# Kernel tuning notes

Hardware: AMD Instinct MI355X
Metric: run time of the kernel (lower is better)

The kernel has to match this reference:

```python
import jax, jax.numpy as jnp
import numpy as np

NEG_INF = jnp.finfo(jnp.float32).min


def setup_inputs() -> dict:
    key = jax.random.key(0)
    ks = jax.random.split(key, 5)
    B, S, D = 2, 2048, 1024
    std = 0.02
    return {
        "x": jax.random.normal(ks[0], (B, S, D), dtype=jnp.float32),
        "attention_mask": jnp.ones((B, S), dtype=jnp.int32),
        "Wq": jax.random.normal(ks[1], (D, D), dtype=jnp.float32) * std,
        "Wk": jax.random.normal(ks[2], (D, D), dtype=jnp.float32) * std,
        "Wv": jax.random.normal(ks[3], (D, D), dtype=jnp.float32) * std,
        "Wo": jax.random.normal(ks[4], (D, D), dtype=jnp.float32) * std,
    }


def reference(x, attention_mask, Wq, Wk, Wv, Wo):
    B, S, D = x.shape
    H = 16
    Hd = D // H
    scale = jnp.float32(np.sqrt(Hd))

    # F.linear uses W @ x^T, i.e. x @ W.T
    def proj(x, W):
        return jnp.einsum('bsd,ed->bse', x, W).reshape(B, S, H, Hd).transpose(0, 2, 1, 3)

    q = proj(x, Wq)  # [B,H,S,Hd]
    k = proj(x, Wk)
    v = proj(x, Wv)

    scores = jnp.einsum('bhqd,bhkd->bhqk', q, k) / scale  # [B,H,S,S]
    causal = jnp.triu(jnp.ones((S, S), dtype=bool), k=1)
    scores = jnp.where(causal[None, None, :, :], NEG_INF, scores)
    key_pad = (attention_mask == 0)[:, None, None, :]  # [B,1,1,S]
    scores = jnp.where(key_pad, NEG_INF, scores)

    attn = jax.nn.softmax(scores, axis=-1)
    out = jnp.einsum('bhqk,bhkd->bhqd', attn, v)  # [B,H,S,Hd]
    out = out.transpose(0, 2, 1, 3).reshape(B, S, D)
    return jnp.einsum('bsd,ed->bse', out, Wo)
```

## Files before the change

kernel.cpp:

```cpp
#include <hip/hip_runtime.h>
#include <hip/hip_bf16.h>

typedef __attribute__((ext_vector_type(8))) short bf16x8;
typedef __attribute__((ext_vector_type(4))) short bf16x4;
typedef __attribute__((ext_vector_type(4))) float f32x4;

#define LOG2E 1.4426950408889634f
#define MBIAS 11.541560327111707f
#define NEGF  -3.0e38f

__device__ __forceinline__ void gl_lds16(const void* g, void* l) {
  __builtin_amdgcn_global_load_lds((const __attribute__((address_space(1))) void*)g,
                                   (__attribute__((address_space(3))) void*)l, 16, 0, 0);
}

__device__ __forceinline__ ushort f2bu(float x) {
  __hip_bfloat16 h = __float2bfloat16(x);
  return *(ushort*)&h;
}

__device__ __forceinline__ unsigned int fbits(float x) {
  union { float f; unsigned int u; } c; c.f = x; return c.u;
}

__global__ __launch_bounds__(256)
void cast_all_k(const float* __restrict__ x, const float* __restrict__ a, const float* __restrict__ b,
                const float* __restrict__ c, const float* __restrict__ d,
                ushort* __restrict__ ox, ushort* __restrict__ oa, ushort* __restrict__ ob,
                ushort* __restrict__ oc, ushort* __restrict__ od) {
  int i = blockIdx.x * 256 + threadIdx.x;
  const float* src; ushort* dst; int j;
  if (i < 1048576) {
    src = x; dst = ox; j = i;
  } else {
    int k = i - 1048576;
    int wsel = k >> 18; j = k & 262143;
    src = wsel == 0 ? a : wsel == 1 ? b : wsel == 2 ? c : d;
    dst = wsel == 0 ? oa : wsel == 1 ? ob : wsel == 2 ? oc : od;
  }
  float4 f = ((const float4*)src)[j];
  ushort4 u;
  u.x = f2bu(f.x); u.y = f2bu(f.y); u.z = f2bu(f.z); u.w = f2bu(f.w);
  ((ushort4*)dst)[j] = u;
}

template<int OUT_BF16>
__device__ __forceinline__ void gemm_body(const ushort* __restrict__ A, const ushort* __restrict__ B,
                                          void* __restrict__ C, int N, int Kd, float scale,
                                          int bm, int bn, ushort (*As)[4096], ushort (*Bs)[4096]) {
  const int t  = threadIdx.x;
  const int l  = t & 63;
  const int w  = t >> 6;
  const int lr = l & 15, lg = l >> 4;
  const int wr = (w >> 1) * 64, wc = (w & 1) * 64;

  auto stage = [&](int buf, int ktE) {
    int idx = t, row = idx >> 2, ch = idx & 3;
    gl_lds16(A + (size_t)(bm + row) * Kd + ktE + ((ch ^ (row & 3)) * 8), &As[buf][idx * 8]);
    gl_lds16(B + (size_t)(bn + row) * Kd + ktE + ((ch ^ (row & 3)) * 8), &Bs[buf][idx * 8]);
    idx = t + 256; row = idx >> 2; ch = idx & 3;
    gl_lds16(A + (size_t)(bm + row) * Kd + ktE + ((ch ^ (row & 3)) * 8), &As[buf][idx * 8]);
    gl_lds16(B + (size_t)(bn + row) * Kd + ktE + ((ch ^ (row & 3)) * 8), &Bs[buf][idx * 8]);
  };

  f32x4 acc[4][4] = {};
  const int nK = Kd >> 5;

  stage(0, 0);
  stage(1, 32);
  int cur = 0;
  for (int k5 = 0; k5 < nK; ++k5) {
    if (k5 + 2 < nK) {
      int nb = cur + 2; if (nb >= 3) nb -= 3;
      stage(nb, (k5 + 2) << 5);
      asm volatile("s_waitcnt vmcnt(8)" ::: "memory");
    } else if (k5 + 1 < nK) {
      asm volatile("s_waitcnt vmcnt(4)" ::: "memory");
    } else {
      asm volatile("s_waitcnt vmcnt(0)" ::: "memory");
    }
    __builtin_amdgcn_s_barrier();

    bf16x8 af[4], bfr[4];
#pragma unroll
    for (int m = 0; m < 4; ++m) {
      int row = wr + m * 16 + lr;
      af[m] = *(const bf16x8*)&As[cur][row * 32 + ((lg ^ (row & 3)) << 3)];
    }
#pragma unroll
    for (int n = 0; n < 4; ++n) {
      int row = wc + n * 16 + lr;
      bfr[n] = *(const bf16x8*)&Bs[cur][row * 32 + ((lg ^ (row & 3)) << 3)];
    }
#pragma unroll
    for (int m = 0; m < 4; ++m)
#pragma unroll
      for (int n = 0; n < 4; ++n)
        acc[m][n] = __builtin_amdgcn_mfma_f32_16x16x32_bf16(af[m], bfr[n], acc[m][n], 0, 0, 0);

    __builtin_amdgcn_s_barrier();
    ++cur; if (cur >= 3) cur -= 3;
  }

#pragma unroll
  for (int m = 0; m < 4; ++m)
#pragma unroll
    for (int n = 0; n < 4; ++n)
#pragma unroll
      for (int j = 0; j < 4; ++j) {
        int row = bm + wr + m * 16 + lg * 4 + j;
        int col = bn + wc + n * 16 + lr;
        float v = acc[m][n][j] * scale;
        if (OUT_BF16) {
          ((ushort*)C)[(size_t)row * N + col] = f2bu(v);
        } else {
          ((float*)C)[(size_t)row * N + col] = v;
        }
      }
}

__global__ __launch_bounds__(256)
void gemm_qkv(const ushort* __restrict__ A, const ushort* __restrict__ Wq, const ushort* __restrict__ Wk,
              const ushort* __restrict__ Wv, ushort* __restrict__ Qo, ushort* __restrict__ Ko,
              ushort* __restrict__ Vo, int Kd) {
  __shared__ __attribute__((aligned(16))) ushort As[3][4096];
  __shared__ __attribute__((aligned(16))) ushort Bs[3][4096];
  int f = blockIdx.x;
  int xcd = f & 7, i = f >> 3;
  int bx = xcd * 4 + (i & 3);
  int by = i >> 2;
  int which = by >> 3;
  const ushort* B = which == 0 ? Wq : which == 1 ? Wk : Wv;
  ushort* C       = which == 0 ? Qo : which == 1 ? Ko : Vo;
  float scale = which == 0 ? 0.125f : 1.0f;
  gemm_body<1>(A, B, C, 1024, Kd, scale, bx * 128, (by & 7) * 128, As, Bs);
}

__global__ __launch_bounds__(256)
void gemm_out64(const ushort* __restrict__ A, const ushort* __restrict__ B, float* __restrict__ C,
                int N, int Kd) {
  __shared__ __attribute__((aligned(16))) ushort As[3][2048];
  __shared__ __attribute__((aligned(16))) ushort Bs[3][4096];
  const int t  = threadIdx.x;
  const int l  = t & 63;
  const int w  = t >> 6;
  const int lr = l & 15, lg = l >> 4;
  const int wr = (w >> 1) * 32, wc = (w & 1) * 64;
  int f = blockIdx.x;
  int xcd = f & 7, i = f >> 3;
  const int bm = (xcd * 8 + (i & 7)) * 64;
  const int bn = (i >> 3) * 128;

  auto stage = [&](int buf, int ktE) {
    int idx = t, row = idx >> 2, ch = idx & 3;
    gl_lds16(A + (size_t)(bm + row) * Kd + ktE + ((ch ^ (row & 3)) * 8), &As[buf][idx * 8]);
    gl_lds16(B + (size_t)(bn + row) * Kd + ktE + ((ch ^ (row & 3)) * 8), &Bs[buf][idx * 8]);
    idx = t + 256; row = idx >> 2; ch = idx & 3;
    gl_lds16(B + (size_t)(bn + row) * Kd + ktE + ((ch ^ (row & 3)) * 8), &Bs[buf][idx * 8]);
  };

  f32x4 acc[2][4] = {};
  const int nK = Kd >> 5;

  stage(0, 0);
  stage(1, 32);
  int cur = 0;
  for (int k5 = 0; k5 < nK; ++k5) {
    if (k5 + 2 < nK) {
      int nb = cur + 2; if (nb >= 3) nb -= 3;
      stage(nb, (k5 + 2) << 5);
      asm volatile("s_waitcnt vmcnt(6)" ::: "memory");
    } else if (k5 + 1 < nK) {
      asm volatile("s_waitcnt vmcnt(3)" ::: "memory");
    } else {
      asm volatile("s_waitcnt vmcnt(0)" ::: "memory");
    }
    __builtin_amdgcn_s_barrier();

    bf16x8 af[2], bfr[4];
#pragma unroll
    for (int m = 0; m < 2; ++m) {
      int row = wr + m * 16 + lr;
      af[m] = *(const bf16x8*)&As[cur][row * 32 + ((lg ^ (row & 3)) << 3)];
    }
#pragma unroll
    for (int n = 0; n < 4; ++n) {
      int row = wc + n * 16 + lr;
      bfr[n] = *(const bf16x8*)&Bs[cur][row * 32 + ((lg ^ (row & 3)) << 3)];
    }
#pragma unroll
    for (int m = 0; m < 2; ++m)
#pragma unroll
      for (int n = 0; n < 4; ++n)
        acc[m][n] = __builtin_amdgcn_mfma_f32_16x16x32_bf16(af[m], bfr[n], acc[m][n], 0, 0, 0);

    __builtin_amdgcn_s_barrier();
    ++cur; if (cur >= 3) cur -= 3;
  }

#pragma unroll
  for (int m = 0; m < 2; ++m)
#pragma unroll
    for (int n = 0; n < 4; ++n)
#pragma unroll
      for (int j = 0; j < 4; ++j) {
        int row = bm + wr + m * 16 + lg * 4 + j;
        int col = bn + wc + n * 16 + lr;
        C[(size_t)row * N + col] = acc[m][n][j];
      }
}

__device__ __forceinline__ void fixed_sm(f32x4 s4[4], bf16x8& pa0_out, bf16x8& pa1_out) {
#pragma unroll
  for (int c = 0; c < 4; ++c)
#pragma unroll
    for (int j = 0; j < 4; ++j)
      s4[c][j] = exp2f(fmaf(s4[c][j], LOG2E, -MBIAS));
  union { bf16x8 v; unsigned int w[4]; } pa0, pa1;
#pragma unroll
  for (int c = 0; c < 2; ++c) {
    pa0.w[2 * c + 0] = __builtin_amdgcn_perm(fbits(s4[c][1]), fbits(s4[c][0]), 0x07060302u);
    pa0.w[2 * c + 1] = __builtin_amdgcn_perm(fbits(s4[c][3]), fbits(s4[c][2]), 0x07060302u);
    pa1.w[2 * c + 0] = __builtin_amdgcn_perm(fbits(s4[c + 2][1]), fbits(s4[c + 2][0]), 0x07060302u);
    pa1.w[2 * c + 1] = __builtin_amdgcn_perm(fbits(s4[c + 2][3]), fbits(s4[c + 2][2]), 0x07060302u);
  }
  pa0_out = pa0.v;
  pa1_out = pa1.v;
}

__global__ __launch_bounds__(512, 4)
void attn_k(const ushort* __restrict__ Q, const ushort* __restrict__ K,
            const ushort* __restrict__ V, const int* __restrict__ mask,
            ushort* __restrict__ O) {
  const int S = 2048, D = 1024;
  __shared__ __attribute__((aligned(16))) ushort Ks[4][4096];
  __shared__ __attribute__((aligned(16))) ushort Vs[4][4096];
  __shared__ unsigned long long Msb[32];

  const int t = threadIdx.x;
  const int l = t & 63, w = t >> 6;
  const int lr = l & 15, lg = l >> 4;

  int f = blockIdx.x;
  int pp = (f >> 3) & 15;
  int ss = ((f >> 8) & 1) ? 15 - pp : pp;
  int bh = (f & 7) | (((f >> 7) & 3) << 3);
  int h = bh & 15, b = bh >> 4;
  const int nt = 2 * ss + 2;
  const int np = ss + 1;
  const int q0 = ss * 128;
  const bool hiW = (w >> 2);
  const int npO = hiW ? np : np - 1;
  const int cdi = w & 3;
  const size_t bS = (size_t)b * S;

  const ushort* qptr = Q + (bS + q0 + w * 16 + lr) * D + h * 64;
  bf16x8 qf0 = *(const bf16x8*)(qptr + lg * 8);
  bf16x8 qf1 = *(const bf16x8*)(qptr + 32 + lg * 8);

  const ushort* Kbh = K + bS * D + h * 64;
  const ushort* Vbh = V + bS * D + h * 64;
  const int* mbase = mask + bS;

  bf16x8 onesf;
#pragma unroll
  for (int i = 0; i < 8; ++i) onesf[i] = (short)0x3F80;

  int koffA[4], koffB[4];
#pragma unroll
  for (int c = 0; c < 4; ++c) {
    int row = c * 16 + lr;
    koffA[c] = row * 64 + ((lg ^ (row & 7)) << 3);
    koffB[c] = row * 64 + (((4 + lg) ^ (row & 7)) << 3);
  }
  int voff[4];
#pragma unroll
  for (int dt = 0; dt < 4; ++dt) voff[dt] = dt * 1024 + lg * 64 + lr * 4;

  for (int kk = w; kk < nt; kk += 8) {
    unsigned long long mb = __ballot(mbase[kk * 64 + l] != 0);
    if (l == 0) Msb[kk] = mb;
  }
  asm volatile("s_waitcnt lgkmcnt(0)" ::: "memory");
  __builtin_amdgcn_sched_barrier(0);

  f32x4 lsum = {0.f, 0.f, 0.f, 0.f};
  f32x4 oE[4] = {}, oO[4] = {};

  auto stage = [&](int p) {
    int s0 = (p & 1) << 1;
    int k0 = 2 * p, k1 = 2 * p + 1;
    { int idx = t; int row = idx >> 3, ch = idx & 7;
      size_t go = (size_t)row * D + ((ch ^ (row & 7)) * 8);
      gl_lds16(Kbh + (size_t)(k0 * 64) * D + go, &Ks[s0][idx * 8]);
      gl_lds16(Kbh + (size_t)(k1 * 64) * D + go, &Ks[s0 + 1][idx * 8]); }
    { int idx = t; int dg = idx >> 7, kq = (idx >> 3) & 15, jj = (idx >> 1) & 3, hf = idx & 1;
      size_t go = (size_t)(kq * 4 + jj) * D + dg * 16 + hf * 8;
      gl_lds16(Vbh + (size_t)(k0 * 64) * D + go, &Vs[s0][idx * 8]);
      gl_lds16(Vbh + (size_t)(k1 * 64) * D + go, &Vs[s0 + 1][idx * 8]); }
  };

  stage(0);
  if (np > 1) stage(1);

  for (int p = 0; p < np; ++p) {
    const int s0 = (p & 1) << 1;
    if (p + 1 < np) asm volatile("s_waitcnt vmcnt(4)" ::: "memory");
    else            asm volatile("s_waitcnt vmcnt(0)" ::: "memory");
    __builtin_amdgcn_s_barrier();

    const bool actO  = (p < npO);
    const bool diagE = (!hiW) && (p == ss);
    const bool diagO = hiW && (p == ss);
    const int cmaxE = diagE ? cdi : 3;
    const int cmaxO = diagO ? cdi : 3;
    unsigned long long mbE = Msb[2 * p];
    unsigned long long mbO = Msb[2 * p + 1];

    f32x4 sE[4], sO[4];
#pragma unroll
    for (int c = 0; c < 4; ++c) {
      if (c <= cmaxE) {
        bf16x8 kf0 = *(const bf16x8*)&Ks[s0][koffA[c]];
        bf16x8 kf1 = *(const bf16x8*)&Ks[s0][koffB[c]];
        f32x4 sc = {0.f, 0.f, 0.f, 0.f};
        sc = __builtin_amdgcn_mfma_f32_16x16x32_bf16(kf0, qf0, sc, 0, 0, 0);
        sc = __builtin_amdgcn_mfma_f32_16x16x32_bf16(kf1, qf1, sc, 0, 0, 0);
        if (diagE && c == cmaxE) {
          int qg = cdi * 16 + lr, kb = c * 16 + lg * 4;
#pragma unroll
          for (int j = 0; j < 4; ++j)
            if (kb + j > qg) sc[j] = NEGF;
        }
        sE[c] = sc;
      } else {
        sE[c] = (f32x4){NEGF, NEGF, NEGF, NEGF};
      }
      if (actO) {
        if (c <= cmaxO) {
          bf16x8 kf0 = *(const bf16x8*)&Ks[s0 + 1][koffA[c]];
          bf16x8 kf1 = *(const bf16x8*)&Ks[s0 + 1][koffB[c]];
          f32x4 sc = {0.f, 0.f, 0.f, 0.f};
          sc = __builtin_amdgcn_mfma_f32_16x16x32_bf16(kf0, qf0, sc, 0, 0, 0);
          sc = __builtin_amdgcn_mfma_f32_16x16x32_bf16(kf1, qf1, sc, 0, 0, 0);
          if (diagO && c == cmaxO) {
            int qg = cdi * 16 + lr, kb = c * 16 + lg * 4;
#pragma unroll
            for (int j = 0; j < 4; ++j)
              if (kb + j > qg) sc[j] = NEGF;
          }
          sO[c] = sc;
        } else {
          sO[c] = (f32x4){NEGF, NEGF, NEGF, NEGF};
        }
      }
    }

    if (~mbE != 0ull) {
#pragma unroll
      for (int c = 0; c < 4; ++c)
#pragma unroll
        for (int j = 0; j < 4; ++j)
          if (!((mbE >> (c * 16 + lg * 4 + j)) & 1)) sE[c][j] = NEGF;
    }
    if (actO && (~mbO != 0ull)) {
#pragma unroll
      for (int c = 0; c < 4; ++c)
#pragma unroll
        for (int j = 0; j < 4; ++j)
          if (!((mbO >> (c * 16 + lg * 4 + j)) & 1)) sO[c][j] = NEGF;
    }

    bf16x8 paE0, paE1;
    fixed_sm(sE, paE0, paE1);
    lsum = __builtin_amdgcn_mfma_f32_16x16x32_bf16(paE0, onesf, lsum, 0, 0, 0);
    lsum = __builtin_amdgcn_mfma_f32_16x16x32_bf16(paE1, onesf, lsum, 0, 0, 0);
#pragma unroll
    for (int dt = 0; dt < 4; ++dt) {
      const __attribute__((address_space(3))) ushort* vp =
          (const __attribute__((address_space(3))) ushort*)&Vs[s0][0] + voff[dt];
      bf16x4 h0, h1, h2, h3;
      asm volatile(
          "ds_read_b64_tr_b16 %0, %4\n\t"
          "ds_read_b64_tr_b16 %1, %4 offset:512\n\t"
          "ds_read_b64_tr_b16 %2, %4 offset:1024\n\t"
          "ds_read_b64_tr_b16 %3, %4 offset:1536\n\t"
          "s_waitcnt lgkmcnt(0)"
          : "=&v"(h0), "=&v"(h1), "=&v"(h2), "=&v"(h3)
          : "v"(vp));
      bf16x8 vb0 = __builtin_shufflevector(h0, h1, 0, 1, 2, 3, 4, 5, 6, 7);
      bf16x8 vb1 = __builtin_shufflevector(h2, h3, 0, 1, 2, 3, 4, 5, 6, 7);
      oE[dt] = __builtin_amdgcn_mfma_f32_16x16x32_bf16(paE0, vb0, oE[dt], 0, 0, 0);
      oE[dt] = __builtin_amdgcn_mfma_f32_16x16x32_bf16(paE1, vb1, oE[dt], 0, 0, 0);
    }

    if (actO) {
      bf16x8 paO0, paO1;
      fixed_sm(sO, paO0, paO1);
      lsum = __builtin_amdgcn_mfma_f32_16x16x32_bf16(paO0, onesf, lsum, 0, 0, 0);
      lsum = __builtin_amdgcn_mfma_f32_16x16x32_bf16(paO1, onesf, lsum, 0, 0, 0);
#pragma unroll
      for (int dt = 0; dt < 4; ++dt) {
        const __attribute__((address_space(3))) ushort* vp =
            (const __attribute__((address_space(3))) ushort*)&Vs[s0 + 1][0] + voff[dt];
        bf16x4 h0, h1, h2, h3;
        asm volatile(
            "ds_read_b64_tr_b16 %0, %4\n\t"
            "ds_read_b64_tr_b16 %1, %4 offset:512\n\t"
            "ds_read_b64_tr_b16 %2, %4 offset:1024\n\t"
            "ds_read_b64_tr_b16 %3, %4 offset:1536\n\t"
            "s_waitcnt lgkmcnt(0)"
            : "=&v"(h0), "=&v"(h1), "=&v"(h2), "=&v"(h3)
            : "v"(vp));
        bf16x8 vb0 = __builtin_shufflevector(h0, h1, 0, 1, 2, 3, 4, 5, 6, 7);
        bf16x8 vb1 = __builtin_shufflevector(h2, h3, 0, 1, 2, 3, 4, 5, 6, 7);
        oO[dt] = __builtin_amdgcn_mfma_f32_16x16x32_bf16(paO0, vb0, oO[dt], 0, 0, 0);
        oO[dt] = __builtin_amdgcn_mfma_f32_16x16x32_bf16(paO1, vb1, oO[dt], 0, 0, 0);
      }
    }

    __builtin_amdgcn_s_barrier();
    if (p + 2 < np) stage(p + 2);
  }

  float iv0 = 1.0f / lsum[0];
  float iv1 = 1.0f / lsum[1];
  float iv2 = 1.0f / lsum[2];
  float iv3 = 1.0f / lsum[3];
#pragma unroll
  for (int dt = 0; dt < 4; ++dt) {
    size_t col = (size_t)h * 64 + dt * 16 + lr;
    size_t r0 = bS + q0 + w * 16 + lg * 4;
    O[(r0 + 0) * D + col] = f2bu((oE[dt][0] + oO[dt][0]) * iv0);
    O[(r0 + 1) * D + col] = f2bu((oE[dt][1] + oO[dt][1]) * iv1);
    O[(r0 + 2) * D + col] = f2bu((oE[dt][2] + oO[dt][2]) * iv2);
    O[(r0 + 3) * D + col] = f2bu((oE[dt][3] + oO[dt][3]) * iv3);
  }
}

extern "C" void kernel_launch(void* const* d_in, const int* in_sizes, int n_in,
                              void* d_out, int out_size, void* d_ws, size_t ws_size,
                              hipStream_t stream) {
  const float* x    = (const float*)d_in[0];
  const int*   mask = (const int*)d_in[1];
  const float* Wq   = (const float*)d_in[2];
  const float* Wk   = (const float*)d_in[3];
  const float* Wv   = (const float*)d_in[4];
  const float* Wo   = (const float*)d_in[5];
  float* out = (float*)d_out;

  const int B = 2, S = 2048, D = 1024;
  const int M = B * S;

  char* ws = (char*)d_ws;
  ushort* xb  = (ushort*)(ws);
  ushort* wqb = (ushort*)(ws + (8ull  << 20));
  ushort* wkb = (ushort*)(ws + (10ull << 20));
  ushort* wvb = (ushort*)(ws + (12ull << 20));
  ushort* wob = (ushort*)(ws + (14ull << 20));
  ushort* Qb  = (ushort*)(ws + (16ull << 20));
  ushort* Kb  = (ushort*)(ws + (24ull << 20));
  ushort* Vb  = (ushort*)(ws + (32ull << 20));
  ushort* AO  = (ushort*)(ws + (40ull << 20));

  cast_all_k<<<8192, 256, 0, stream>>>(x, Wq, Wk, Wv, Wo, xb, wqb, wkb, wvb, wob);

  gemm_qkv<<<768, 256, 0, stream>>>(xb, wqb, wkb, wvb, Qb, Kb, Vb, D);

  attn_k<<<512, 512, 0, stream>>>(Qb, Kb, Vb, mask, AO);

  gemm_out64<<<512, 256, 0, stream>>>(AO, wob, out, D, D);
}
```

Before: 112.2 us.

## Replace QKV GEMM with 256x256-tile, 512-thread, BK=64 double-buffered kernel

The fused QKV projection GEMM moves from 128x128 tiles with 256 threads, BK=32 and triple buffering to 256x256 tiles with 512 threads, BK=64 and double buffering. Each wave now computes a 128x64 sub-tile, which raises operand reuse per LDS load and halves the number of barriers per K step. The LDS swizzle is widened to 8 chunks. The trade-offs are only 192 blocks on a GPU with many CUs, 128 KB of LDS per block, a full vmcnt(0) wait each iteration with less prefetch depth, and higher register pressure.

```diff
diff --git a/kernel.cpp b/kernel.cpp
--- a/kernel.cpp
+++ b/kernel.cpp
@@ -44,96 +44,84 @@
   ((ushort4*)dst)[j] = u;
 }
 
-template<int OUT_BF16>
-__device__ __forceinline__ void gemm_body(const ushort* __restrict__ A, const ushort* __restrict__ B,
-                                          void* __restrict__ C, int N, int Kd, float scale,
-                                          int bm, int bn, ushort (*As)[4096], ushort (*Bs)[4096]) {
-  const int t  = threadIdx.x;
-  const int l  = t & 63;
-  const int w  = t >> 6;
+__global__ __launch_bounds__(512, 2)
+void gemm_qkv256(const ushort* __restrict__ A, const ushort* __restrict__ Wq,
+                 const ushort* __restrict__ Wk, const ushort* __restrict__ Wv,
+                 ushort* __restrict__ Qo, ushort* __restrict__ Ko, ushort* __restrict__ Vo) {
+  __shared__ __attribute__((aligned(16))) ushort As[2][16384];
+  __shared__ __attribute__((aligned(16))) ushort Bs[2][16384];
+  const int Kd = 1024, N = 1024;
+  const int t = threadIdx.x;
+  const int l = t & 63;
+  const int w = t >> 6;
   const int lr = l & 15, lg = l >> 4;
-  const int wr = (w >> 1) * 64, wc = (w & 1) * 64;
+  const int wm = (w >> 2) * 128;
+  const int wn = (w & 3) * 64;
+
+  int f = blockIdx.x;
+  int xcd = f & 7, g = f >> 3;
+  int bx = xcd * 2 + (g & 1);
+  int h2 = g >> 1;
+  int which = h2 >> 2;
+  int by = h2 & 3;
+  const ushort* Bw = which == 0 ? Wq : which == 1 ? Wk : Wv;
+  ushort* C        = which == 0 ? Qo : which == 1 ? Ko : Vo;
+  const float scale = which == 0 ? 0.125f : 1.0f;
+  const int bm = bx * 256, bn = by * 256;
 
   auto stage = [&](int buf, int ktE) {
-    int idx = t, row = idx >> 2, ch = idx & 3;
-    gl_lds16(A + (size_t)(bm + row) * Kd + ktE + ((ch ^ (row & 3)) * 8), &As[buf][idx * 8]);
-    gl_lds16(B + (size_t)(bn + row) * Kd + ktE + ((ch ^ (row & 3)) * 8), &Bs[buf][idx * 8]);
-    idx = t + 256; row = idx >> 2; ch = idx & 3;
-    gl_lds16(A + (size_t)(bm + row) * Kd + ktE + ((ch ^ (row & 3)) * 8), &As[buf][idx * 8]);
-    gl_lds16(B + (size_t)(bn + row) * Kd + ktE + ((ch ^ (row & 3)) * 8), &Bs[buf][idx * 8]);
+#pragma unroll
+    for (int i = 0; i < 4; ++i) {
+      int idx = t + 512 * i;
+      int row = idx >> 3, ch = idx & 7;
+      gl_lds16(A  + (size_t)(bm + row) * Kd + ktE + ((ch ^ (row & 7)) * 8), &As[buf][idx * 8]);
+      gl_lds16(Bw + (size_t)(bn + row) * Kd + ktE + ((ch ^ (row & 7)) * 8), &Bs[buf][idx * 8]);
+    }
   };
 
-  f32x4 acc[4][4] = {};
-  const int nK = Kd >> 5;
+  f32x4 acc[8][4] = {};
 
   stage(0, 0);
-  stage(1, 32);
+  asm volatile("s_waitcnt vmcnt(0)" ::: "memory");
+  __builtin_amdgcn_s_barrier();
+
   int cur = 0;
-  for (int k5 = 0; k5 < nK; ++k5) {
-    if (k5 + 2 < nK) {
-      int nb = cur + 2; if (nb >= 3) nb -= 3;
-      stage(nb, (k5 + 2) << 5);
-      asm volatile("s_waitcnt vmcnt(8)" ::: "memory");
-    } else if (k5 + 1 < nK) {
-      asm volatile("s_waitcnt vmcnt(4)" ::: "memory");
-    } else {
-      asm volatile("s_waitcnt vmcnt(0)" ::: "memory");
-    }
+  for (int k5 = 0; k5 < 16; ++k5) {
+    if (k5 + 1 < 16) stage(cur ^ 1, (k5 + 1) << 6);
+
+#pragma unroll
+    for (int ks = 0; ks < 2; ++ks) {
+      bf16x8 bfr[4];
+#pragma unroll
+      for (int n = 0; n < 4; ++n) {
+        int row = wn + n * 16 + lr;
+        bfr[n] = *(const bf16x8*)&Bs[cur][row * 64 + (((ks * 4 + lg) ^ (row & 7)) << 3)];
+      }
+#pragma unroll
+      for (int m = 0; m < 8; ++m) {
+        int row = wm + m * 16 + lr;
+        bf16x8 af = *(const bf16x8*)&As[cur][row * 64 + (((ks * 4 + lg) ^ (row & 7)) << 3)];
+#pragma unroll
+        for (int n = 0; n < 4; ++n)
+          acc[m][n] = __builtin_amdgcn_mfma_f32_16x16x32_bf16(af, bfr[n], acc[m][n], 0, 0, 0);
+      }
+    }
+
+    asm volatile("s_waitcnt vmcnt(0)" ::: "memory");
     __builtin_amdgcn_s_barrier();
-
-    bf16x8 af[4], bfr[4];
-#pragma unroll
-    for (int m = 0; m < 4; ++m) {
-      int row = wr + m * 16 + lr;
-      af[m] = *(const bf16x8*)&As[cur][row * 32 + ((lg ^ (row & 3)) << 3)];
-    }
-#pragma unroll
-    for (int n = 0; n < 4; ++n) {
-      int row = wc + n * 16 + lr;
-      bfr[n] = *(const bf16x8*)&Bs[cur][row * 32 + ((lg ^ (row & 3)) << 3)];
-    }
-#pragma unroll
-    for (int m = 0; m < 4; ++m)
-#pragma unroll
-      for (int n = 0; n < 4; ++n)
-        acc[m][n] = __builtin_amdgcn_mfma_f32_16x16x32_bf16(af[m], bfr[n], acc[m][n], 0, 0, 0);
-
-    __builtin_amdgcn_s_barrier();
-    ++cur; if (cur >= 3) cur -= 3;
-  }
-
-#pragma unroll
-  for (int m = 0; m < 4; ++m)
+    cur ^= 1;
+  }
+
+#pragma unroll
+  for (int m = 0; m < 8; ++m)
 #pragma unroll
     for (int n = 0; n < 4; ++n)
 #pragma unroll
       for (int j = 0; j < 4; ++j) {
-        int row = bm + wr + m * 16 + lg * 4 + j;
-        int col = bn + wc + n * 16 + lr;
-        float v = acc[m][n][j] * scale;
-        if (OUT_BF16) {
-          ((ushort*)C)[(size_t)row * N + col] = f2bu(v);
-        } else {
-          ((float*)C)[(size_t)row * N + col] = v;
-        }
-      }
-}
-
-__global__ __launch_bounds__(256)
-void gemm_qkv(const ushort* __restrict__ A, const ushort* __restrict__ Wq, const ushort* __restrict__ Wk,
-              const ushort* __restrict__ Wv, ushort* __restrict__ Qo, ushort* __restrict__ Ko,
-              ushort* __restrict__ Vo, int Kd) {
-  __shared__ __attribute__((aligned(16))) ushort As[3][4096];
-  __shared__ __attribute__((aligned(16))) ushort Bs[3][4096];
-  int f = blockIdx.x;
-  int xcd = f & 7, i = f >> 3;
-  int bx = xcd * 4 + (i & 3);
-  int by = i >> 2;
-  int which = by >> 3;
-  const ushort* B = which == 0 ? Wq : which == 1 ? Wk : Wv;
-  ushort* C       = which == 0 ? Qo : which == 1 ? Ko : Vo;
-  float scale = which == 0 ? 0.125f : 1.0f;
-  gemm_body<1>(A, B, C, 1024, Kd, scale, bx * 128, (by & 7) * 128, As, Bs);
+        int row = bm + wm + m * 16 + lg * 4 + j;
+        int col = bn + wn + n * 16 + lr;
+        C[(size_t)row * N + col] = f2bu(acc[m][n][j] * scale);
+      }
 }
 
 __global__ __launch_bounds__(256)
@@ -465,7 +453,7 @@
 
   cast_all_k<<<8192, 256, 0, stream>>>(x, Wq, Wk, Wv, Wo, xb, wqb, wkb, wvb, wob);
 
-  gemm_qkv<<<768, 256, 0, stream>>>(xb, wqb, wkb, wvb, Qb, Kb, Vb, D);
+  gemm_qkv256<<<192, 512, 0, stream>>>(xb, wqb, wkb, wvb, Qb, Kb, Vb);
 
   attn_k<<<512, 512, 0, stream>>>(Qb, Kb, Vb, mask, AO);
 
```

After: 118.1 us. 5.3% more time.
